# Optimization experiments

Hardware: AMD Instinct MI355X
Metric: run time of the kernel (lower is better)

Reference implementation:

```python
import jax, jax.numpy as jnp
import numpy as np

N = 50000        # nodes
E = 1500000      # edges
D = 128          # hidden_dim
L = 3            # layers_mp (t = 0..L-1)
RBAR = 1         # cfg.rbar -> delay = max(k - RBAR, 0)
EPS = 0.0        # GIN epsilon (not trainable)


def setup_inputs() -> dict:
    key = jax.random.key(0)
    ks = jax.random.split(key, 6)
    x = jax.random.normal(ks[0], (N, D), dtype=jnp.float32)
    edge_index = jax.random.randint(ks[1], (2, E), 0, N)          # [2, E] src/dst
    edge_attr = jax.random.randint(ks[2], (E,), 0, L)             # relation id k-1 in {0..L-1}
    # per-layer mlp_s: Linear(D, D) + ReLU
    Ws_s = jax.random.normal(ks[3], (L, D, D), dtype=jnp.float32) / np.float32(np.sqrt(D))
    bs_s = jnp.zeros((L, D), dtype=jnp.float32)
    # per-layer, per-relation mlp_k[k-1]: Linear(D, D) + ReLU (layer t uses k = 1..t+1)
    Ws_k = jax.random.normal(ks[4], (L, L, D, D), dtype=jnp.float32) / np.float32(np.sqrt(D))
    bs_k = jnp.zeros((L, L, D), dtype=jnp.float32)
    return dict(x=x, Ws_s=Ws_s, bs_s=bs_s, Ws_k=Ws_k, bs_k=bs_k,
                edge_index=edge_index, edge_attr=edge_attr)


def reference(x, Ws_s, bs_s, Ws_k, bs_k, edge_index, edge_attr):
    src, dst = edge_index[0], edge_index[1]
    n = x.shape[0]
    xs = []
    for t in range(L):
        xs.append(x)
        out = None
        for k in range(1, t + 2):
            delay = max(k - RBAR, 0)
            h_src = xs[t - delay]                       # delayed history for relation k
            # edge-type-grouped scatter-add: mask edges of relation k, gather, segment-sum
            mask = (edge_attr == (k - 1))
            msg = jnp.where(mask[:, None], h_src[src], jnp.float32(0.0))   # [E, D]
            agg = jax.ops.segment_sum(msg, dst, num_segments=n)            # [N, D]
            h = jax.nn.relu(agg @ Ws_k[t, k - 1] + bs_k[t, k - 1])         # mlp_k[k-1]
            out = h if out is None else out + h
        # self term: (1 + eps) * mlp_s(x); nn_post is identity (empty Sequential)
        out = out + (1.0 + EPS) * jax.nn.relu(x @ Ws_s[t] + bs_s[t])
        # outer loop: ReLU, dropout(p=0, eval), residual
        x = xs[-1] + jax.nn.relu(out)
    return x
```

## Files before the change

kernel.cpp:

```cpp
#include <hip/hip_runtime.h>

#define NN 50000
#define NE 1500000
#define DD 128
#define NRANGE ((NN + 255) / 256)
#define NBUCK (3 * NRANGE)
#define BINB 256
#define CHUNK ((NE + BINB - 1) / BINB)
#define NH2 (NBUCK * BINB)

typedef __attribute__((ext_vector_type(8))) short short8;
typedef __attribute__((ext_vector_type(4))) float f32x4;

__device__ __forceinline__ ushort f2b(float x) {
    uint u = __float_as_uint(x);
    u += 0x7FFFu + ((u >> 16) & 1u);
    return (ushort)(u >> 16);
}
__device__ __forceinline__ float b2f(ushort b) {
    return __uint_as_float(((uint)b) << 16);
}

__global__ __launch_bounds__(256) void scan_block(
    const int* __restrict__ cnt, int* __restrict__ ptr, int* __restrict__ part, int n)
{
    __shared__ int s[256];
    int i = blockIdx.x * 256 + threadIdx.x;
    int v = (i < n) ? cnt[i] : 0;
    s[threadIdx.x] = v;
    __syncthreads();
    #pragma unroll
    for (int off = 1; off < 256; off <<= 1) {
        int t = (threadIdx.x >= off) ? s[threadIdx.x - off] : 0;
        __syncthreads();
        s[threadIdx.x] += t;
        __syncthreads();
    }
    if (i < n) ptr[i] = s[threadIdx.x] - v;
    if (threadIdx.x == 255) part[blockIdx.x] = s[255];
}

__global__ void scan_partials(int* __restrict__ part, int nb)
{
    int lane = threadIdx.x;
    int run = 0;
    for (int base = 0; base < nb; base += 64) {
        int i = base + lane;
        int v = (i < nb) ? part[i] : 0;
        int x = v;
        #pragma unroll
        for (int off = 1; off < 64; off <<= 1) {
            int t = __shfl_up(x, off);
            if (lane >= off) x += t;
        }
        if (i < nb) part[i] = run + x - v;
        run += __shfl(x, 63);
    }
}

__global__ __launch_bounds__(256) void scan_add(
    int* __restrict__ ptr, const int* __restrict__ part, int n)
{
    int i = blockIdx.x * 256 + threadIdx.x;
    if (i >= n) return;
    ptr[i] += part[blockIdx.x];
}

__global__ __launch_bounds__(256) void histB(
    const int* __restrict__ dst, const int* __restrict__ attr, int* __restrict__ hist2)
{
    __shared__ int lh[NBUCK];
    int tid = threadIdx.x, blk = blockIdx.x;
    for (int i = tid; i < NBUCK; i += 256) lh[i] = 0;
    __syncthreads();
    int lo = blk * CHUNK, hi = lo + CHUNK; if (hi > NE) hi = NE;
    for (int e = lo + tid; e < hi; e += 256)
        atomicAdd(&lh[attr[e] * NRANGE + (dst[e] >> 8)], 1);
    __syncthreads();
    for (int i = tid; i < NBUCK; i += 256) hist2[i * BINB + blk] = lh[i];
}

__global__ __launch_bounds__(256) void binB(
    const int* __restrict__ src, const int* __restrict__ dst, const int* __restrict__ attr,
    const int* __restrict__ off2, uint* __restrict__ binned)
{
    __shared__ int lc[NBUCK];
    int tid = threadIdx.x, blk = blockIdx.x;
    for (int i = tid; i < NBUCK; i += 256) lc[i] = off2[i * BINB + blk];
    __syncthreads();
    int lo = blk * CHUNK, hi = lo + CHUNK; if (hi > NE) hi = NE;
    for (int e = lo + tid; e < hi; e += 256) {
        int d = dst[e];
        int b = attr[e] * NRANGE + (d >> 8);
        int pos = atomicAdd(&lc[b], 1);
        binned[pos] = (uint)src[e] | ((uint)(d & 255) << 16);
    }
}

__global__ __launch_bounds__(256) void bucket_finalize(
    const uint* __restrict__ binned, const int* __restrict__ off2,
    int* __restrict__ ptr, ushort* __restrict__ ssrc)
{
    __shared__ int lh[256];
    __shared__ int sc[256];
    __shared__ int cur[256];
    int b = blockIdx.x, tid = threadIdx.x;
    int rel = b / NRANGE, r0 = (b % NRANGE) << 8;
    int nloc = NN - r0; if (nloc > 256) nloc = 256;
    int lo = off2[b * BINB];
    int hi = (b + 1 < NBUCK) ? off2[(b + 1) * BINB] : NE;
    lh[tid] = 0;
    __syncthreads();
    for (int e = lo + tid; e < hi; e += 256)
        atomicAdd(&lh[(binned[e] >> 16) & 255], 1);
    __syncthreads();
    int v = lh[tid];
    sc[tid] = v;
    __syncthreads();
    #pragma unroll
    for (int off = 1; off < 256; off <<= 1) {
        int t = (tid >= off) ? sc[tid - off] : 0;
        __syncthreads();
        sc[tid] += t;
        __syncthreads();
    }
    int excl = lo + sc[tid] - v;
    if (tid < nloc) ptr[rel * NN + r0 + tid] = excl;
    cur[tid] = excl;
    if (b == NBUCK - 1 && tid == 0) ptr[3 * NN] = NE;
    __syncthreads();
    for (int e = lo + tid; e < hi; e += 256) {
        uint p = binned[e];
        int pos = atomicAdd(&cur[(p >> 16) & 255], 1);
        ssrc[pos] = (ushort)(p & 0xFFFFu);
    }
}

__global__ __launch_bounds__(256) void prep_w(
    const float* __restrict__ Ws_s, const float* __restrict__ Ws_k, ushort* __restrict__ wt)
{
    int i = blockIdx.x * 256 + threadIdx.x;
    if (i >= 9 * 4096) return;
    int m = i >> 12;
    int f = (i & 4095) * 4;
    int k = f >> 7, n = f & 127;
    const int tk[6] = {0, 3, 4, 6, 7, 8};
    const float* W = (m < 3) ? (Ws_s + (size_t)m * 16384)
                             : (Ws_k + (size_t)tk[m - 3] * 16384);
    float4 v = *(const float4*)(W + (size_t)k * DD + n);
    ushort* o = wt + (size_t)m * 16384 + k;
    o[(size_t)(n + 0) * DD] = f2b(v.x);
    o[(size_t)(n + 1) * DD] = f2b(v.y);
    o[(size_t)(n + 2) * DD] = f2b(v.z);
    o[(size_t)(n + 3) * DD] = f2b(v.w);
}

__global__ __launch_bounds__(256) void to_bf16(
    const float* __restrict__ x, ushort* __restrict__ xb)
{
    int i = blockIdx.x * 256 + threadIdx.x;
    if (i >= NN * DD / 4) return;
    float4 v = ((const float4*)x)[i];
    ushort4 o;
    o.x = f2b(v.x); o.y = f2b(v.y); o.z = f2b(v.z); o.w = f2b(v.w);
    ((ushort4*)xb)[i] = o;
}

__global__ __launch_bounds__(256) void gather_multi(
    const ushort* __restrict__ h,
    const int* __restrict__ ptr, const ushort* __restrict__ ssrc,
    ushort* __restrict__ a0, ushort* __restrict__ a1, ushort* __restrict__ a2)
{
    int rel = blockIdx.y;
    ushort* agg = (rel == 0) ? a0 : ((rel == 1) ? a1 : a2);

    int n = blockIdx.x * 4 + (threadIdx.x >> 6);
    if (n >= NN) return;
    int lane = threadIdx.x & 63;
    const int* p = ptr + rel * NN + n;
    int s0 = __builtin_amdgcn_readfirstlane(p[0]);
    int s1 = __builtin_amdgcn_readfirstlane(p[1]);
    float a0f = 0.f, a1f = 0.f, c0f = 0.f, c1f = 0.f;
    int e = s0;
    for (; e + 8 <= s1; e += 8) {
        int idx[8];
        #pragma unroll
        for (int j = 0; j < 8; ++j) idx[j] = ssrc[e + j];
        uint v[8];
        #pragma unroll
        for (int j = 0; j < 8; ++j)
            v[j] = ((const uint*)(h + (size_t)idx[j] * DD))[lane];
        #pragma unroll
        for (int j = 0; j < 8; j += 2) {
            a0f += b2f((ushort)(v[j] & 0xFFFFu));     a1f += b2f((ushort)(v[j] >> 16));
            c0f += b2f((ushort)(v[j + 1] & 0xFFFFu)); c1f += b2f((ushort)(v[j + 1] >> 16));
        }
    }
    for (; e + 4 <= s1; e += 4) {
        int i0 = ssrc[e], i1 = ssrc[e + 1], i2 = ssrc[e + 2], i3 = ssrc[e + 3];
        uint v0 = ((const uint*)(h + (size_t)i0 * DD))[lane];
        uint v1 = ((const uint*)(h + (size_t)i1 * DD))[lane];
        uint v2 = ((const uint*)(h + (size_t)i2 * DD))[lane];
        uint v3 = ((const uint*)(h + (size_t)i3 * DD))[lane];
        a0f += b2f((ushort)(v0 & 0xFFFFu)); a1f += b2f((ushort)(v0 >> 16));
        c0f += b2f((ushort)(v1 & 0xFFFFu)); c1f += b2f((ushort)(v1 >> 16));
        a0f += b2f((ushort)(v2 & 0xFFFFu)); a1f += b2f((ushort)(v2 >> 16));
        c0f += b2f((ushort)(v3 & 0xFFFFu)); c1f += b2f((ushort)(v3 >> 16));
    }
    for (; e < s1; ++e) {
        int s = ssrc[e];
        uint v = ((const uint*)(h + (size_t)s * DD))[lane];
        a0f += b2f((ushort)(v & 0xFFFFu)); a1f += b2f((ushort)(v >> 16));
    }
    a0f += c0f; a1f += c1f;
    uint o = (uint)f2b(a0f) | ((uint)f2b(a1f) << 16);
    ((uint*)(agg + (size_t)n * DD))[lane] = o;
}

template<int NSRC, int WRITEB>
__global__ __launch_bounds__(256) void layer_mm(
    const ushort* __restrict__ s0, const ushort* __restrict__ s1,
    const ushort* __restrict__ s2, const ushort* __restrict__ s3,
    const ushort* __restrict__ w0, const ushort* __restrict__ w1,
    const ushort* __restrict__ w2, const ushort* __restrict__ w3,
    const float* __restrict__ b0, const float* __restrict__ b1,
    const float* __restrict__ b2, const float* __restrict__ b3,
    const float* __restrict__ xold, float* __restrict__ xnew, ushort* __restrict__ xbnew)
{
    __shared__ ushort Atile[64 * 128];
    const int tid  = threadIdx.x;
    const int wave = tid >> 6, lane = tid & 63;
    const int row0 = blockIdx.x * 64;

    const ushort* srcs[4] = { s0, s1, s2, s3 };
    const ushort* wts[4]  = { w0, w1, w2, w3 };
    const float*  bss[4]  = { b0, b1, b2, b3 };

    float facc[4][2][4];
    #pragma unroll
    for (int rt = 0; rt < 4; ++rt)
        #pragma unroll
        for (int ct = 0; ct < 2; ++ct)
            #pragma unroll
            for (int q = 0; q < 4; ++q) facc[rt][ct][q] = 0.f;

    #pragma unroll
    for (int sidx = 0; sidx < NSRC; ++sidx) {
        const ushort* S = srcs[sidx];
        const ushort* W = wts[sidx];

        __syncthreads();
        for (int i = tid; i < 1024; i += 256) {
            int r = i >> 4, c = i & 15;
            int gr = row0 + r;
            uint4 v = make_uint4(0, 0, 0, 0);
            if (gr < NN) v = ((const uint4*)(S + (size_t)gr * DD))[c];
            int byte = ((r << 8) + (c << 4)) ^ ((r & 7) << 4);
            *((uint4*)((char*)Atile + byte)) = v;
        }
        short8 bfr[2][4];
        #pragma unroll
        for (int ct = 0; ct < 2; ++ct)
            #pragma unroll
            for (int ks = 0; ks < 4; ++ks) {
                int col = (wave << 5) + (ct << 4) + (lane & 15);
                int kb  = (ks << 5) + ((lane >> 4) << 3);
                bfr[ct][ks] = *(const short8*)(W + (size_t)col * DD + kb);
            }
        __syncthreads();

        f32x4 c[4][2];
        #pragma unroll
        for (int rt = 0; rt < 4; ++rt)
            #pragma unroll
            for (int ct = 0; ct < 2; ++ct) c[rt][ct] = (f32x4)(0.f);

        #pragma unroll
        for (int rt = 0; rt < 4; ++rt) {
            int row = (rt << 4) + (lane & 15);
            #pragma unroll
            for (int ks = 0; ks < 4; ++ks) {
                int byte = ((row << 8) + (ks << 6) + ((lane >> 4) << 4)) ^ ((row & 7) << 4);
                short8 a = *((const short8*)((const char*)Atile + byte));
                c[rt][0] = __builtin_amdgcn_mfma_f32_16x16x32_bf16(a, bfr[0][ks], c[rt][0], 0, 0, 0);
                c[rt][1] = __builtin_amdgcn_mfma_f32_16x16x32_bf16(a, bfr[1][ks], c[rt][1], 0, 0, 0);
            }
        }

        const float* B = bss[sidx];
        #pragma unroll
        for (int ct = 0; ct < 2; ++ct) {
            float bb = B[(wave << 5) + (ct << 4) + (lane & 15)];
            #pragma unroll
            for (int rt = 0; rt < 4; ++rt)
                #pragma unroll
                for (int q = 0; q < 4; ++q) {
                    float v = c[rt][ct][q] + bb;
                    facc[rt][ct][q] += v > 0.f ? v : 0.f;
                }
        }
    }

    #pragma unroll
    for (int rt = 0; rt < 4; ++rt)
        #pragma unroll
        for (int q = 0; q < 4; ++q) {
            int row = row0 + (rt << 4) + ((lane >> 4) << 2) + q;
            if (row >= NN) continue;
            #pragma unroll
            for (int ct = 0; ct < 2; ++ct) {
                int col = (wave << 5) + (ct << 4) + (lane & 15);
                size_t off = (size_t)row * DD + col;
                float v = facc[rt][ct][q] + xold[off];
                xnew[off] = v;
                if (WRITEB) xbnew[off] = f2b(v);
            }
        }
}

extern "C" void kernel_launch(void* const* d_in, const int* in_sizes, int n_in,
                              void* d_out, int out_size, void* d_ws, size_t ws_size,
                              hipStream_t stream) {
    const float* x0   = (const float*)d_in[0];
    const float* Ws_s = (const float*)d_in[1];
    const float* bs_s = (const float*)d_in[2];
    const float* Ws_k = (const float*)d_in[3];
    const float* bs_k = (const float*)d_in[4];
    const int*   src  = (const int*)d_in[5];
    const int*   dst  = src + NE;
    const int*   attr = (const int*)d_in[6];
    float* out = (float*)d_out;

    float*  x1   = (float*)d_ws;
    ushort* xb0  = (ushort*)(x1 + (size_t)NN * DD);
    ushort* xb1  = xb0 + (size_t)NN * DD;
    ushort* xb2  = xb1 + (size_t)NN * DD;
    ushort* P0   = xb2 + (size_t)NN * DD;
    ushort* P1   = P0 + (size_t)NN * DD;
    ushort* P2   = P1 + (size_t)NN * DD;
    ushort* P3   = P2 + (size_t)NN * DD;
    ushort* wtb  = P3 + (size_t)NN * DD;
    int* ptr    = (int*)(wtb + 9 * 16384);
    int* part2  = ptr + 3 * NN + 1;
    ushort* ssrc = (ushort*)(part2 + 1024);
    int* hist2  = (int*)P1;
    int* off2   = (int*)P2;
    uint* binned = (uint*)P3;

    const int gGemm = (NN + 63) / 64;
    const int gGath = (NN + 3) / 4;
    const int gConv = (NN * DD / 4 + 255) / 256;
    const int NB2 = (NH2 + 255) / 256;

    auto wt = [&](int m) { return wtb + (size_t)m * 16384; };
    auto bk = [&](int t, int k) { return bs_k + ((size_t)t * 3 + k) * DD; };

    histB<<<BINB, 256, 0, stream>>>(dst, attr, hist2);
    scan_block<<<NB2, 256, 0, stream>>>(hist2, off2, part2, NH2);
    scan_partials<<<1, 64, 0, stream>>>(part2, NB2);
    scan_add<<<NB2, 256, 0, stream>>>(off2, part2, NH2);
    binB<<<BINB, 256, 0, stream>>>(src, dst, attr, off2, binned);
    bucket_finalize<<<NBUCK, 256, 0, stream>>>(binned, off2, ptr, ssrc);
    prep_w<<<144, 256, 0, stream>>>(Ws_s, Ws_k, wtb);
    to_bf16<<<gConv, 256, 0, stream>>>(x0, xb0);

    gather_multi<<<dim3(gGath, 3), 256, 0, stream>>>(xb0, ptr, ssrc, P0, P1, P3);
    layer_mm<2, 1><<<gGemm, 256, 0, stream>>>(
        xb0, P0, nullptr, nullptr,
        wt(0), wt(3), nullptr, nullptr,
        bs_s, bk(0, 0), nullptr, nullptr,
        x0, x1, xb1);

    gather_multi<<<dim3(gGath, 2), 256, 0, stream>>>(xb1, ptr, ssrc, P0, P2, nullptr);
    layer_mm<3, 1><<<gGemm, 256, 0, stream>>>(
        xb1, P0, P1, nullptr,
        wt(1), wt(4), wt(5), nullptr,
        bs_s + DD, bk(1, 0), bk(1, 1), nullptr,
        x1, out, xb2);

    gather_multi<<<dim3(gGath, 1), 256, 0, stream>>>(xb2, ptr, ssrc, P0, nullptr, nullptr);
    layer_mm<4, 0><<<gGemm, 256, 0, stream>>>(
        xb2, P0, P2, P3,
        wt(2), wt(6), wt(7), wt(8),
        bs_s + 2 * DD, bk(2, 0), bk(2, 1), bk(2, 2),
        out, out, nullptr);
}
```

Baseline: 298.5 us.

## Merge prep kernels, defer relation gathers to use delayed histories, prefetch edge indices

Fuses histogram, x-to-bf16 conversion and weight prep into a single launch, so three small kernels become one and their work can overlap. The relation-1/2 aggregations are no longer computed early from xb0 and kept in scratch. Each layer's gather instead reads the delayed history buffers (xb0, xb1) directly, which frees one aggregation buffer and repacks the workspace layout. The gather loop also software-prefetches the next 8 source indices while the current rows are loaded. The rescheduled gathers do the same total work but spread it across layers.

```diff
diff --git a/kernel.cpp b/kernel.cpp
--- a/kernel.cpp
+++ b/kernel.cpp
@@ -8,6 +8,7 @@
 #define BINB 256
 #define CHUNK ((NE + BINB - 1) / BINB)
 #define NH2 (NBUCK * BINB)
+#define GCONV ((NN * DD / 4 + 255) / 256)
 
 typedef __attribute__((ext_vector_type(8))) short short8;
 typedef __attribute__((ext_vector_type(4))) float f32x4;
@@ -66,18 +67,46 @@
     ptr[i] += part[blockIdx.x];
 }
 
-__global__ __launch_bounds__(256) void histB(
-    const int* __restrict__ dst, const int* __restrict__ attr, int* __restrict__ hist2)
+__global__ __launch_bounds__(256) void prep_all(
+    const int* __restrict__ dst, const int* __restrict__ attr, int* __restrict__ hist2,
+    const float* __restrict__ x, ushort* __restrict__ xb,
+    const float* __restrict__ Ws_s, const float* __restrict__ Ws_k, ushort* __restrict__ wt)
 {
     __shared__ int lh[NBUCK];
-    int tid = threadIdx.x, blk = blockIdx.x;
-    for (int i = tid; i < NBUCK; i += 256) lh[i] = 0;
-    __syncthreads();
-    int lo = blk * CHUNK, hi = lo + CHUNK; if (hi > NE) hi = NE;
-    for (int e = lo + tid; e < hi; e += 256)
-        atomicAdd(&lh[attr[e] * NRANGE + (dst[e] >> 8)], 1);
-    __syncthreads();
-    for (int i = tid; i < NBUCK; i += 256) hist2[i * BINB + blk] = lh[i];
+    int b = blockIdx.x, tid = threadIdx.x;
+    if (b < BINB) {
+        for (int i = tid; i < NBUCK; i += 256) lh[i] = 0;
+        __syncthreads();
+        int lo = b * CHUNK, hi = lo + CHUNK; if (hi > NE) hi = NE;
+        for (int e = lo + tid; e < hi; e += 256)
+            atomicAdd(&lh[attr[e] * NRANGE + (dst[e] >> 8)], 1);
+        __syncthreads();
+        for (int i = tid; i < NBUCK; i += 256) hist2[i * BINB + b] = lh[i];
+    } else if (b < BINB + GCONV) {
+        int i = (b - BINB) * 256 + tid;
+        if (i < NN * DD / 4) {
+            float4 v = ((const float4*)x)[i];
+            ushort4 o;
+            o.x = f2b(v.x); o.y = f2b(v.y); o.z = f2b(v.z); o.w = f2b(v.w);
+            ((ushort4*)xb)[i] = o;
+        }
+    } else {
+        int i = (b - BINB - GCONV) * 256 + tid;
+        if (i < 9 * 4096) {
+            int m = i >> 12;
+            int f = (i & 4095) * 4;
+            int k = f >> 7, n = f & 127;
+            const int tk[6] = {0, 3, 4, 6, 7, 8};
+            const float* W = (m < 3) ? (Ws_s + (size_t)m * 16384)
+                                     : (Ws_k + (size_t)tk[m - 3] * 16384);
+            float4 v = *(const float4*)(W + (size_t)k * DD + n);
+            ushort* o = wt + (size_t)m * 16384 + k;
+            o[(size_t)(n + 0) * DD] = f2b(v.x);
+            o[(size_t)(n + 1) * DD] = f2b(v.y);
+            o[(size_t)(n + 2) * DD] = f2b(v.z);
+            o[(size_t)(n + 3) * DD] = f2b(v.w);
+        }
+    }
 }
 
 __global__ __launch_bounds__(256) void binB(
@@ -136,43 +165,15 @@
     }
 }
 
-__global__ __launch_bounds__(256) void prep_w(
-    const float* __restrict__ Ws_s, const float* __restrict__ Ws_k, ushort* __restrict__ wt)
-{
-    int i = blockIdx.x * 256 + threadIdx.x;
-    if (i >= 9 * 4096) return;
-    int m = i >> 12;
-    int f = (i & 4095) * 4;
-    int k = f >> 7, n = f & 127;
-    const int tk[6] = {0, 3, 4, 6, 7, 8};
-    const float* W = (m < 3) ? (Ws_s + (size_t)m * 16384)
-                             : (Ws_k + (size_t)tk[m - 3] * 16384);
-    float4 v = *(const float4*)(W + (size_t)k * DD + n);
-    ushort* o = wt + (size_t)m * 16384 + k;
-    o[(size_t)(n + 0) * DD] = f2b(v.x);
-    o[(size_t)(n + 1) * DD] = f2b(v.y);
-    o[(size_t)(n + 2) * DD] = f2b(v.z);
-    o[(size_t)(n + 3) * DD] = f2b(v.w);
-}
-
-__global__ __launch_bounds__(256) void to_bf16(
-    const float* __restrict__ x, ushort* __restrict__ xb)
-{
-    int i = blockIdx.x * 256 + threadIdx.x;
-    if (i >= NN * DD / 4) return;
-    float4 v = ((const float4*)x)[i];
-    ushort4 o;
-    o.x = f2b(v.x); o.y = f2b(v.y); o.z = f2b(v.z); o.w = f2b(v.w);
-    ((ushort4*)xb)[i] = o;
-}
-
 __global__ __launch_bounds__(256) void gather_multi(
-    const ushort* __restrict__ h,
+    const ushort* __restrict__ h0, const ushort* __restrict__ h1,
+    const ushort* __restrict__ h2,
     const int* __restrict__ ptr, const ushort* __restrict__ ssrc,
     ushort* __restrict__ a0, ushort* __restrict__ a1, ushort* __restrict__ a2)
 {
     int rel = blockIdx.y;
-    ushort* agg = (rel == 0) ? a0 : ((rel == 1) ? a1 : a2);
+    const ushort* h = (rel == 0) ? h0 : ((rel == 1) ? h1 : h2);
+    ushort* agg     = (rel == 0) ? a0 : ((rel == 1) ? a1 : a2);
 
     int n = blockIdx.x * 4 + (threadIdx.x >> 6);
     if (n >= NN) return;
@@ -180,21 +181,31 @@
     const int* p = ptr + rel * NN + n;
     int s0 = __builtin_amdgcn_readfirstlane(p[0]);
     int s1 = __builtin_amdgcn_readfirstlane(p[1]);
-    float a0f = 0.f, a1f = 0.f, c0f = 0.f, c1f = 0.f;
+    float A0 = 0.f, A1 = 0.f, C0 = 0.f, C1 = 0.f;
     int e = s0;
-    for (; e + 8 <= s1; e += 8) {
-        int idx[8];
+    int idx[8];
+    bool have = (e + 8 <= s1);
+    if (have) {
         #pragma unroll
         for (int j = 0; j < 8; ++j) idx[j] = ssrc[e + j];
+    }
+    while (have) {
         uint v[8];
         #pragma unroll
         for (int j = 0; j < 8; ++j)
             v[j] = ((const uint*)(h + (size_t)idx[j] * DD))[lane];
+        int e2 = e + 8;
+        bool nxt = (e2 + 8 <= s1);
+        if (nxt) {
+            #pragma unroll
+            for (int j = 0; j < 8; ++j) idx[j] = ssrc[e2 + j];
+        }
         #pragma unroll
         for (int j = 0; j < 8; j += 2) {
-            a0f += b2f((ushort)(v[j] & 0xFFFFu));     a1f += b2f((ushort)(v[j] >> 16));
-            c0f += b2f((ushort)(v[j + 1] & 0xFFFFu)); c1f += b2f((ushort)(v[j + 1] >> 16));
-        }
+            A0 += b2f((ushort)(v[j] & 0xFFFFu));     A1 += b2f((ushort)(v[j] >> 16));
+            C0 += b2f((ushort)(v[j + 1] & 0xFFFFu)); C1 += b2f((ushort)(v[j + 1] >> 16));
+        }
+        e = e2; have = nxt;
     }
     for (; e + 4 <= s1; e += 4) {
         int i0 = ssrc[e], i1 = ssrc[e + 1], i2 = ssrc[e + 2], i3 = ssrc[e + 3];
@@ -202,18 +213,18 @@
         uint v1 = ((const uint*)(h + (size_t)i1 * DD))[lane];
         uint v2 = ((const uint*)(h + (size_t)i2 * DD))[lane];
         uint v3 = ((const uint*)(h + (size_t)i3 * DD))[lane];
-        a0f += b2f((ushort)(v0 & 0xFFFFu)); a1f += b2f((ushort)(v0 >> 16));
-        c0f += b2f((ushort)(v1 & 0xFFFFu)); c1f += b2f((ushort)(v1 >> 16));
-        a0f += b2f((ushort)(v2 & 0xFFFFu)); a1f += b2f((ushort)(v2 >> 16));
-        c0f += b2f((ushort)(v3 & 0xFFFFu)); c1f += b2f((ushort)(v3 >> 16));
+        A0 += b2f((ushort)(v0 & 0xFFFFu)); A1 += b2f((ushort)(v0 >> 16));
+        C0 += b2f((ushort)(v1 & 0xFFFFu)); C1 += b2f((ushort)(v1 >> 16));
+        A0 += b2f((ushort)(v2 & 0xFFFFu)); A1 += b2f((ushort)(v2 >> 16));
+        C0 += b2f((ushort)(v3 & 0xFFFFu)); C1 += b2f((ushort)(v3 >> 16));
     }
     for (; e < s1; ++e) {
         int s = ssrc[e];
         uint v = ((const uint*)(h + (size_t)s * DD))[lane];
-        a0f += b2f((ushort)(v & 0xFFFFu)); a1f += b2f((ushort)(v >> 16));
-    }
-    a0f += c0f; a1f += c1f;
-    uint o = (uint)f2b(a0f) | ((uint)f2b(a1f) << 16);
+        A0 += b2f((ushort)(v & 0xFFFFu)); A1 += b2f((ushort)(v >> 16));
+    }
+    A0 += C0; A1 += C1;
+    uint o = (uint)f2b(A0) | ((uint)f2b(A1) << 16);
     ((uint*)(agg + (size_t)n * DD))[lane] = o;
 }
 
@@ -338,49 +349,49 @@
     ushort* P0   = xb2 + (size_t)NN * DD;
     ushort* P1   = P0 + (size_t)NN * DD;
     ushort* P2   = P1 + (size_t)NN * DD;
-    ushort* P3   = P2 + (size_t)NN * DD;
-    ushort* wtb  = P3 + (size_t)NN * DD;
+    ushort* wtb  = P2 + (size_t)NN * DD;
     int* ptr    = (int*)(wtb + 9 * 16384);
     int* part2  = ptr + 3 * NN + 1;
     ushort* ssrc = (ushort*)(part2 + 1024);
+    uint* binned = (uint*)P0;
     int* hist2  = (int*)P1;
-    int* off2   = (int*)P2;
-    uint* binned = (uint*)P3;
+    int* off2   = hist2 + NH2;
 
     const int gGemm = (NN + 63) / 64;
     const int gGath = (NN + 3) / 4;
-    const int gConv = (NN * DD / 4 + 255) / 256;
     const int NB2 = (NH2 + 255) / 256;
 
     auto wt = [&](int m) { return wtb + (size_t)m * 16384; };
     auto bk = [&](int t, int k) { return bs_k + ((size_t)t * 3 + k) * DD; };
 
-    histB<<<BINB, 256, 0, stream>>>(dst, attr, hist2);
+    prep_all<<<BINB + GCONV + 144, 256, 0, stream>>>(
+        dst, attr, hist2, x0, xb0, Ws_s, Ws_k, wtb);
     scan_block<<<NB2, 256, 0, stream>>>(hist2, off2, part2, NH2);
     scan_partials<<<1, 64, 0, stream>>>(part2, NB2);
     scan_add<<<NB2, 256, 0, stream>>>(off2, part2, NH2);
     binB<<<BINB, 256, 0, stream>>>(src, dst, attr, off2, binned);
     bucket_finalize<<<NBUCK, 256, 0, stream>>>(binned, off2, ptr, ssrc);
-    prep_w<<<144, 256, 0, stream>>>(Ws_s, Ws_k, wtb);
-    to_bf16<<<gConv, 256, 0, stream>>>(x0, xb0);
-
-    gather_multi<<<dim3(gGath, 3), 256, 0, stream>>>(xb0, ptr, ssrc, P0, P1, P3);
+
+    gather_multi<<<dim3(gGath, 1), 256, 0, stream>>>(
+        xb0, nullptr, nullptr, ptr, ssrc, P0, nullptr, nullptr);
     layer_mm<2, 1><<<gGemm, 256, 0, stream>>>(
         xb0, P0, nullptr, nullptr,
         wt(0), wt(3), nullptr, nullptr,
         bs_s, bk(0, 0), nullptr, nullptr,
         x0, x1, xb1);
 
-    gather_multi<<<dim3(gGath, 2), 256, 0, stream>>>(xb1, ptr, ssrc, P0, P2, nullptr);
+    gather_multi<<<dim3(gGath, 2), 256, 0, stream>>>(
+        xb1, xb0, nullptr, ptr, ssrc, P0, P1, nullptr);
     layer_mm<3, 1><<<gGemm, 256, 0, stream>>>(
         xb1, P0, P1, nullptr,
         wt(1), wt(4), wt(5), nullptr,
         bs_s + DD, bk(1, 0), bk(1, 1), nullptr,
         x1, out, xb2);
 
-    gather_multi<<<dim3(gGath, 1), 256, 0, stream>>>(xb2, ptr, ssrc, P0, nullptr, nullptr);
+    gather_multi<<<dim3(gGath, 3), 256, 0, stream>>>(
+        xb2, xb1, xb0, ptr, ssrc, P0, P1, P2);
     layer_mm<4, 0><<<gGemm, 256, 0, stream>>>(
-        xb2, P0, P2, P3,
+        xb2, P0, P1, P2,
         wt(2), wt(6), wt(7), wt(8),
         bs_s + 2 * DD, bk(2, 0), bk(2, 1), bk(2, 2),
         out, out, nullptr);
```

After: 295.2 us. About the same (-1.1%).
